# Kernel optimization log

Measured on AMD Instinct MI355X. Metric: run time of the kernel, lower is better.

## Reference

```python
import jax, jax.numpy as jnp
import numpy as np

E, B, D, H, Z = 8, 16384, 512, 512, 64   # experts, batch, input_dim, hidden, latent
NHID = 2                                 # num_mlp_layers - 1 hidden-to-hidden layers


def setup_inputs() -> dict:
    key = jax.random.key(0)
    ks = jax.random.split(key, 12)

    def w(k, shape, fan_in):
        return (jax.random.normal(k, shape, jnp.float32) / np.sqrt(fan_in)).astype(jnp.float32)

    return {
        "x": jax.random.normal(ks[0], (B, D), jnp.float32),
        "eps": jax.random.normal(ks[1], (B, Z), jnp.float32),
        # stacked per-expert parameters (leading axis E)
        "enc_in_w": w(ks[2], (E, D, H), D), "enc_in_b": jnp.zeros((E, H), jnp.float32),
        "enc_hid_w": w(ks[3], (E, NHID, H, H), H), "enc_hid_b": jnp.zeros((E, NHID, H), jnp.float32),
        "mu_w": w(ks[4], (E, H, Z), H), "mu_b": jnp.zeros((E, Z), jnp.float32),
        "lv_w": w(ks[5], (E, H, Z), H), "lv_b": jnp.zeros((E, Z), jnp.float32),
        "dec_in_w": w(ks[6], (E, Z, H), Z), "dec_in_b": jnp.zeros((E, H), jnp.float32),
        "dec_hid_w": w(ks[7], (E, NHID, H, H), H), "dec_hid_b": jnp.zeros((E, NHID, H), jnp.float32),
        "dec_out_w": w(ks[8], (E, H, D), H), "dec_out_b": jnp.zeros((E, D), jnp.float32),
    }


def _moe_forward(x, eps, enc_in_w, enc_in_b, enc_hid_w, enc_hid_b,
                 mu_w, mu_b, lv_w, lv_b,
                 dec_in_w, dec_in_b, dec_hid_w, dec_hid_b, dec_out_w, dec_out_b):
    # ---- every expert tries the problem (dense, all experts over full batch) ----
    h = jax.nn.relu(jnp.einsum('bd,edh->ebh', x, enc_in_w) + enc_in_b[:, None, :])
    for i in range(NHID):
        h = jax.nn.relu(jnp.einsum('ebh,ehk->ebk', h, enc_hid_w[:, i]) + enc_hid_b[:, i, None, :])
    mu = jnp.einsum('ebh,ehz->ebz', h, mu_w) + mu_b[:, None, :]          # [E,B,Z]
    logvar = jnp.einsum('ebh,ehz->ebz', h, lv_w) + lv_b[:, None, :]       # [E,B,Z]
    z = mu + jnp.exp(0.5 * logvar) * eps[None, :, :]                      # reparameterize
    g = jax.nn.relu(jnp.einsum('ebz,ezh->ebh', z, dec_in_w) + dec_in_b[:, None, :])
    for i in range(NHID):
        g = jax.nn.relu(jnp.einsum('ebh,ehk->ebk', g, dec_hid_w[:, i]) + dec_hid_b[:, i, None, :])
    xhat = jnp.einsum('ebh,ehd->ebd', g, dec_out_w) + dec_out_b[:, None, :]  # [E,B,D]

    # ---- per-sample recon loss, pick best expert (torch.min over experts) ----
    recon = jnp.mean((xhat - x[None, :, :]) ** 2, axis=-1)                # [E,B]
    expert_idx = jnp.argmin(recon, axis=0)                                # [B]

    # ---- sparse_others: single fused gather instead of python loop ----
    bi = jnp.arange(x.shape[0])
    return mu[expert_idx, bi], logvar[expert_idx, bi], xhat[expert_idx, bi]


def reference(x, eps, enc_in_w, enc_in_b, enc_hid_w, enc_hid_b,
              mu_w, mu_b, lv_w, lv_b,
              dec_in_w, dec_in_b, dec_hid_w, dec_hid_b, dec_out_w, dec_out_b):
    return _moe_forward(x, eps, enc_in_w, enc_in_b, enc_hid_w, enc_hid_b,
                        mu_w, mu_b, lv_w, lv_b,
                        dec_in_w, dec_in_b, dec_hid_w, dec_hid_b, dec_out_w, dec_out_b)
```

## Files before the change

### kernel.cpp

```cpp
#include <hip/hip_runtime.h>
#include <cstdint>

#define Eexp 8
#define Bb   16384
#define Dd   512
#define Hh   512
#define Zz   64

typedef _Float16 f16x8 __attribute__((ext_vector_type(8)));
typedef float    f32x4 __attribute__((ext_vector_type(4)));

#define OFF_ENCIN  0
#define OFF_HID0   524288
#define OFF_HID1   1048576
#define OFF_HEADS  1572864
#define OFF_DECIN  1703936
#define OFF_DHID0  1769472
#define OFF_DHID1  2293760
#define OFF_DECOUT 2818048
#define PEREXP     3342336
#define WT_TOTAL   (8 * (size_t)PEREXP)

#define GLL16(g, l) __builtin_amdgcn_global_load_lds( \
    (const __attribute__((address_space(1))) void*)(g), \
    (__attribute__((address_space(3))) void*)(l), 16, 0, 0)

template<bool TR>
__global__ __launch_bounds__(256)
void fmsplit(const float* __restrict__ src, _Float16* __restrict__ dst,
             int KTOT, int inner, long sStride, long dStride)
{
    __shared__ float t[64][65];
    const int e  = blockIdx.z;
    const int o0 = blockIdx.x * 64;
    const int k0 = blockIdx.y * 64;
    const float* S = src + (size_t)e * sStride;
    _Float16*    D = dst + (size_t)e * dStride;
    const int tid = threadIdx.x;
    const int rr = tid >> 4, c4 = (tid & 15) * 4;
    #pragma unroll
    for (int p = 0; p < 4; ++p) {
        const int r = rr + p * 16;
        const float4 v = *reinterpret_cast<const float4*>(
            S + (size_t)(TR ? (k0 + r) : (o0 + r)) * inner + (TR ? o0 : k0) + c4);
        t[r][c4 + 0] = v.x; t[r][c4 + 1] = v.y;
        t[r][c4 + 2] = v.z; t[r][c4 + 3] = v.w;
    }
    __syncthreads();
    const int lane = tid & 63, wid = tid >> 6;
    const int KB = KTOT >> 5;
    #pragma unroll
    for (int p = 0; p < 2; ++p) {
        const int g  = wid * 2 + p;
        const int ot = g >> 1, kb = g & 1;
        const int rI = ot * 16 + (lane & 15);
        const int kI = kb * 32 + (lane >> 4) * 8;
        f16x8 hv, lv;
        #pragma unroll
        for (int j = 0; j < 8; ++j) {
            const float v = TR ? t[kI + j][rI] : t[rI][kI + j];
            const _Float16 h = (_Float16)v;
            hv[j] = h; lv[j] = (_Float16)(v - (float)h);
        }
        const size_t base = ((size_t)((o0 >> 4) + ot) * KB + (k0 >> 5) + kb) * 1024;
        *reinterpret_cast<f16x8*>(D + base + lane * 8)       = hv;
        *reinterpret_cast<f16x8*>(D + base + 512 + lane * 8) = lv;
    }
}

__global__ __launch_bounds__(256)
void zfm_kernel(const float* __restrict__ mu, const float* __restrict__ lv,
                const float* __restrict__ eps, _Float16* __restrict__ zfm)
{
    __shared__ float t[64][65];
    const int r0 = blockIdx.x * 64;
    const int tid = threadIdx.x, rr = tid >> 4, c4 = (tid & 15) * 4;
    #pragma unroll
    for (int p = 0; p < 4; ++p) {
        const int r = rr + p * 16;
        const size_t o = (size_t)(r0 + r) * 64 + c4;
        const float4 m = *reinterpret_cast<const float4*>(mu + o);
        const float4 l = *reinterpret_cast<const float4*>(lv + o);
        const float4 e = *reinterpret_cast<const float4*>(eps + o);
        t[r][c4 + 0] = m.x + expf(0.5f * l.x) * e.x;
        t[r][c4 + 1] = m.y + expf(0.5f * l.y) * e.y;
        t[r][c4 + 2] = m.z + expf(0.5f * l.z) * e.z;
        t[r][c4 + 3] = m.w + expf(0.5f * l.w) * e.w;
    }
    __syncthreads();
    const int lane = tid & 63, wid = tid >> 6;
    #pragma unroll
    for (int p = 0; p < 2; ++p) {
        const int g  = wid * 2 + p;
        const int ot = g >> 1, kb = g & 1;
        const int rI = ot * 16 + (lane & 15);
        const int kI = kb * 32 + (lane >> 4) * 8;
        f16x8 hv, lvv;
        #pragma unroll
        for (int j = 0; j < 8; ++j) {
            const float v = t[rI][kI + j];
            const _Float16 h = (_Float16)v;
            hv[j] = h; lvv[j] = (_Float16)(v - (float)h);
        }
        const size_t base = ((size_t)((r0 >> 4) + ot) * 2 + kb) * 1024;
        *reinterpret_cast<f16x8*>(zfm + base + lane * 8)       = hv;
        *reinterpret_cast<f16x8*>(zfm + base + 512 + lane * 8) = lvv;
    }
}

template<int KA, int MODE>
__global__ __launch_bounds__(256, 2)
void gemm9(const _Float16* __restrict__ Afm, const _Float16* __restrict__ Wfm,
           const float* __restrict__ bias0, const float* __restrict__ bias1,
           float* __restrict__ Cf, float* __restrict__ Cf1,
           _Float16* __restrict__ Cfm, const float* __restrict__ Xin,
           float* __restrict__ rec8)
{
    constexpr bool BIG = (MODE != 2);
    constexpr int MF  = BIG ? 4 : 2;
    constexpr int KB  = KA / 32;
    constexpr int NT  = KB;
    constexpr int ACH = BIG ? 16 : 8;
    constexpr int GPW = ACH / 4;
    constexpr int VC  = GPW + 8;
    __shared__ __align__(16) uint8_t smem[BIG ? 32768 : 16384];
    _Float16* ring = reinterpret_cast<_Float16*>(smem);

    const int bid = blockIdx.x;
    int bx, by;
    if (BIG) { const int idx = bid >> 3; bx = (bid & 7) * 16 + (idx >> 2); by = idx & 3; }
    else     { bx = (bid & 7) * 32 + (bid >> 3); by = 0; }

    const int lane = threadIdx.x & 63, wid = threadIdx.x >> 6;
    const int wr = wid >> 1, wc = wid & 1;
    const int row0 = bx * (BIG ? 128 : 64);
    const int col0 = by * 128;
    const int ct0  = (BIG ? (col0 >> 4) : 0) + wc * 4;

    const _Float16* aSrc[GPW];
    #pragma unroll
    for (int p = 0; p < GPW; ++p) {
        const int q = wid * GPW + p;
        aSrc[p] = Afm + (size_t)((row0 >> 4) + (q >> 1)) * KB * 1024
                      + (q & 1) * 512 + lane * 8;
    }
    const _Float16* wSrc[8];
    #pragma unroll
    for (int i = 0; i < 8; ++i)
        wSrc[i] = Wfm + (size_t)(ct0 + (i >> 1)) * KB * 1024
                      + (i & 1) * 512 + lane * 8;

    f32x4 acc[MF][4];
    #pragma unroll
    for (int i = 0; i < MF; ++i)
        #pragma unroll
        for (int j = 0; j < 4; ++j) acc[i][j] = {0.f, 0.f, 0.f, 0.f};

    f16x8 wA[4][2], wB[4][2];

#define STAGE_A(buf)                                                         \
    { _Pragma("unroll")                                                      \
      for (int p = 0; p < GPW; ++p) {                                        \
          GLL16(aSrc[p], ring + (buf) * (ACH * 512) + (wid * GPW + p) * 512);\
          aSrc[p] += 1024;                                                   \
      } }

#define LOAD_W(dst)                                                          \
    { _Pragma("unroll")                                                      \
      for (int i = 0; i < 8; ++i) {                                          \
          dst[i >> 1][i & 1] = *reinterpret_cast<const f16x8*>(wSrc[i]);     \
          wSrc[i] += 1024;                                                   \
      } }

    STAGE_A(0) LOAD_W(wA)
    STAGE_A(1) LOAD_W(wB)

#define ITER(t, buf, wset)                                                   \
    {                                                                        \
        if ((t) + 1 < NT) { asm volatile("s_waitcnt vmcnt(%0)" :: "i"(VC) : "memory"); } \
        else              { asm volatile("s_waitcnt vmcnt(0)" ::: "memory"); } \
        __builtin_amdgcn_s_barrier();                                        \
        asm volatile("" ::: "memory");                                       \
        f16x8 ah[MF], al[MF];                                                \
        _Pragma("unroll")                                                    \
        for (int mf = 0; mf < MF; ++mf) {                                    \
            const int q = (wr * MF + mf) * 2;                                \
            ah[mf] = *reinterpret_cast<const f16x8*>(                        \
                ring + (buf) * (ACH * 512) + q * 512 + lane * 8);            \
            al[mf] = *reinterpret_cast<const f16x8*>(                        \
                ring + (buf) * (ACH * 512) + q * 512 + 512 + lane * 8);      \
        }                                                                    \
        __builtin_amdgcn_s_setprio(1);                                       \
        _Pragma("unroll")                                                    \
        for (int mf = 0; mf < MF; ++mf)                                      \
            _Pragma("unroll")                                                \
            for (int nf = 0; nf < 4; ++nf) {                                 \
                acc[mf][nf] = __builtin_amdgcn_mfma_f32_16x16x32_f16(        \
                    ah[mf], wset[nf][0], acc[mf][nf], 0, 0, 0);              \
                acc[mf][nf] = __builtin_amdgcn_mfma_f32_16x16x32_f16(        \
                    ah[mf], wset[nf][1], acc[mf][nf], 0, 0, 0);              \
                acc[mf][nf] = __builtin_amdgcn_mfma_f32_16x16x32_f16(        \
                    al[mf], wset[nf][0], acc[mf][nf], 0, 0, 0);              \
            }                                                                \
        __builtin_amdgcn_s_setprio(0);                                       \
        if ((t) + 2 < NT) LOAD_W(wset)                                       \
        asm volatile("" ::: "memory");                                       \
        __builtin_amdgcn_s_barrier();                                        \
        asm volatile("" ::: "memory");                                       \
        if ((t) + 2 < NT) STAGE_A(buf)                                       \
    }

    for (int t = 0; t < NT; t += 2) {
        ITER(t,     0, wA)
        ITER(t + 1, 1, wB)
    }
#undef ITER
#undef LOAD_W
#undef STAGE_A

    if constexpr (MODE == 0) {
        uint32_t* sb = reinterpret_cast<uint32_t*>(smem);
        #pragma unroll
        for (int ph = 0; ph < 2; ++ph) {
            if (wc == ph) {
                #pragma unroll
                for (int nf = 0; nf < 4; ++nf) {
                    const int c_l = nf * 16 + (lane & 15);
                    const float bv = bias0[col0 + ph * 64 + c_l];
                    #pragma unroll
                    for (int mf = 0; mf < 4; ++mf)
                        #pragma unroll
                        for (int j = 0; j < 4; ++j) {
                            const int r_l = wr * 64 + mf * 16 + (lane >> 4) * 4 + j;
                            const float v = fmaxf(acc[mf][nf][j] + bv, 0.f);
                            const _Float16 h = (_Float16)v;
                            const _Float16 lo = (_Float16)(v - (float)h);
                            const uint32_t pk =
                                (uint32_t)__builtin_bit_cast(uint16_t, h) |
                                ((uint32_t)__builtin_bit_cast(uint16_t, lo) << 16);
                            sb[r_l * 64 + (((c_l >> 2) ^ (r_l & 15)) << 2) + (c_l & 3)] = pk;
                        }
                }
            }
            __syncthreads();
            {
                #pragma unroll
                for (int i = 0; i < 4; ++i) {
                    const int q = wid * 4 + i;
                    const int T_l = q >> 1, kb_l = q & 1;
                    const int r_l = T_l * 16 + (lane & 15);
                    const int cb  = kb_l * 32 + (lane >> 4) * 8;
                    uint32_t u[8];
                    #pragma unroll
                    for (int jb = 0; jb < 2; ++jb) {
                        const int chunk = ((cb >> 2) + jb) ^ (r_l & 15);
                        const uint32_t* pp = &sb[r_l * 64 + chunk * 4];
                        u[jb*4+0] = pp[0]; u[jb*4+1] = pp[1];
                        u[jb*4+2] = pp[2]; u[jb*4+3] = pp[3];
                    }
                    f16x8 hv, lvv;
                    #pragma unroll
                    for (int j = 0; j < 8; ++j) {
                        hv[j]  = __builtin_bit_cast(_Float16, (uint16_t)(u[j] & 0xffff));
                        lvv[j] = __builtin_bit_cast(_Float16, (uint16_t)(u[j] >> 16));
                    }
                    const size_t base =
                        ((size_t)((row0 >> 4) + T_l) * 16 +
                         ((col0 + ph * 64) >> 5) + kb_l) * 1024;
                    *reinterpret_cast<f16x8*>(Cfm + base + lane * 8)       = hv;
                    *reinterpret_cast<f16x8*>(Cfm + base + 512 + lane * 8) = lvv;
                }
            }
            __syncthreads();
        }
    } else if constexpr (MODE == 1) {
        float rsum[4][4];
        #pragma unroll
        for (int mf = 0; mf < 4; ++mf)
            #pragma unroll
            for (int j = 0; j < 4; ++j) rsum[mf][j] = 0.f;
        #pragma unroll
        for (int nf = 0; nf < 4; ++nf) {
            const int col = col0 + wc * 64 + nf * 16 + (lane & 15);
            const float bv = bias0[col];
            #pragma unroll
            for (int mf = 0; mf < 4; ++mf)
                #pragma unroll
                for (int j = 0; j < 4; ++j) {
                    const int row = row0 + wr * 64 + mf * 16 + (lane >> 4) * 4 + j;
                    const float v = acc[mf][nf][j] + bv;
                    Cf[(size_t)row * 512 + col] = v;
                    const float d = v - Xin[(size_t)row * 512 + col];
                    rsum[mf][j] += d * d;
                }
        }
        #pragma unroll
        for (int mf = 0; mf < 4; ++mf)
            #pragma unroll
            for (int j = 0; j < 4; ++j) {
                float s = rsum[mf][j];
                s += __shfl_xor(s, 1); s += __shfl_xor(s, 2);
                s += __shfl_xor(s, 4); s += __shfl_xor(s, 8);
                if ((lane & 15) == 0) {
                    const int row = row0 + wr * 64 + mf * 16 + (lane >> 4) * 4 + j;
                    rec8[(size_t)(by * 2 + wc) * Bb + row] = s;
                }
            }
    } else {
        #pragma unroll
        for (int nf = 0; nf < 4; ++nf) {
            const int c_h = wc * 64 + nf * 16 + (lane & 15);
            const float bv = (c_h < 64) ? bias0[c_h] : bias1[c_h - 64];
            float* CP = (c_h < 64) ? Cf : Cf1;
            const int c = c_h & 63;
            #pragma unroll
            for (int mf = 0; mf < MF; ++mf)
                #pragma unroll
                for (int j = 0; j < 4; ++j) {
                    const int row = row0 + wr * 32 + mf * 16 + (lane >> 4) * 4 + j;
                    CP[(size_t)row * 64 + c] = acc[mf][nf][j] + bv;
                }
        }
    }
}

__global__ __launch_bounds__(256)
void select_kernel(const float* __restrict__ rec8, float* __restrict__ best,
                   const float* __restrict__ mu_e, const float* __restrict__ lv_e,
                   const float* __restrict__ xhat,
                   float* __restrict__ out_mu, float* __restrict__ out_lv,
                   float* __restrict__ out_xh, int isFirst)
{
    const int wave = threadIdx.x >> 6;
    const int lane = threadIdx.x & 63;
    const int row  = blockIdx.x * 4 + wave;
    float r = 0.f;
    #pragma unroll
    for (int p = 0; p < 8; ++p) r += rec8[(size_t)p * Bb + row];
    r *= (1.0f / 512.0f);
    const bool cond = isFirst || (r < best[row]);
    if (cond) {
        if (lane == 0) best[row] = r;
        out_mu[(size_t)row * Zz + lane] = mu_e[(size_t)row * Zz + lane];
        out_lv[(size_t)row * Zz + lane] = lv_e[(size_t)row * Zz + lane];
        const float4* src = reinterpret_cast<const float4*>(&xhat[(size_t)row * Dd]);
        float4*       dst = reinterpret_cast<float4*>(&out_xh[(size_t)row * Dd]);
        dst[lane]      = src[lane];
        dst[lane + 64] = src[lane + 64];
    }
}

extern "C" void kernel_launch(void* const* d_in, const int* in_sizes, int n_in,
                              void* d_out, int out_size, void* d_ws, size_t ws_size,
                              hipStream_t stream)
{
    const float* x         = (const float*)d_in[0];
    const float* eps       = (const float*)d_in[1];
    const float* enc_in_w  = (const float*)d_in[2];
    const float* enc_in_b  = (const float*)d_in[3];
    const float* enc_hid_w = (const float*)d_in[4];
    const float* enc_hid_b = (const float*)d_in[5];
    const float* mu_w      = (const float*)d_in[6];
    const float* mu_b      = (const float*)d_in[7];
    const float* lv_w      = (const float*)d_in[8];
    const float* lv_b      = (const float*)d_in[9];
    const float* dec_in_w  = (const float*)d_in[10];
    const float* dec_in_b  = (const float*)d_in[11];
    const float* dec_hid_w = (const float*)d_in[12];
    const float* dec_hid_b = (const float*)d_in[13];
    const float* dec_out_w = (const float*)d_in[14];
    const float* dec_out_b = (const float*)d_in[15];

    const size_t FM = (size_t)Bb * 512 * 2;
    const size_t BZ = (size_t)Bb * 64;

    _Float16* wt  = (_Float16*)d_ws;
    _Float16* xfm = wt + WT_TOTAL;
    _Float16* afm = xfm + FM;
    _Float16* bfm = afm + FM;
    _Float16* zfm = bfm + FM;
    float* fbase  = (float*)(zfm + (size_t)Bb * 64 * 2);
    float* xhat   = fbase;
    float* mu_e   = xhat + (size_t)Bb * 512;
    float* lv_e   = mu_e + BZ;
    float* rec8   = lv_e + BZ;
    float* best   = rec8 + (size_t)8 * Bb;

    float* out_mu = (float*)d_out;
    float* out_lv = out_mu + (size_t)Bb * Zz;
    float* out_xh = out_lv + (size_t)Bb * Zz;

    const dim3 blk(256);

    fmsplit<true ><<<dim3(8, 8, 8), blk, 0, stream>>>(enc_in_w,           wt + OFF_ENCIN,  512, 512, 262144, PEREXP);
    fmsplit<true ><<<dim3(8, 8, 8), blk, 0, stream>>>(enc_hid_w,          wt + OFF_HID0,   512, 512, 524288, PEREXP);
    fmsplit<true ><<<dim3(8, 8, 8), blk, 0, stream>>>(enc_hid_w + 262144, wt + OFF_HID1,   512, 512, 524288, PEREXP);
    fmsplit<true ><<<dim3(1, 8, 8), blk, 0, stream>>>(mu_w,               wt + OFF_HEADS,  512,  64,  32768, PEREXP);
    fmsplit<true ><<<dim3(1, 8, 8), blk, 0, stream>>>(lv_w,        wt + OFF_HEADS + 65536, 512,  64,  32768, PEREXP);
    fmsplit<true ><<<dim3(8, 1, 8), blk, 0, stream>>>(dec_in_w,           wt + OFF_DECIN,   64, 512,  32768, PEREXP);
    fmsplit<true ><<<dim3(8, 8, 8), blk, 0, stream>>>(dec_hid_w,          wt + OFF_DHID0,  512, 512, 524288, PEREXP);
    fmsplit<true ><<<dim3(8, 8, 8), blk, 0, stream>>>(dec_hid_w + 262144, wt + OFF_DHID1,  512, 512, 524288, PEREXP);
    fmsplit<true ><<<dim3(8, 8, 8), blk, 0, stream>>>(dec_out_w,          wt + OFF_DECOUT, 512, 512, 262144, PEREXP);
    fmsplit<false><<<dim3(256, 8, 1), blk, 0, stream>>>(x,                xfm,             512, 512, 0, 0);

    const dim3 g512(512), g256(256), gRow(Bb / 4), gZ(Bb / 64);

    for (int e = 0; e < Eexp; ++e) {
        const _Float16* we = wt + (size_t)e * PEREXP;
        gemm9<512, 0><<<g512, blk, 0, stream>>>(
            xfm, we + OFF_ENCIN, enc_in_b + (size_t)e * Hh, nullptr,
            nullptr, nullptr, afm, nullptr, nullptr);
        gemm9<512, 0><<<g512, blk, 0, stream>>>(
            afm, we + OFF_HID0, enc_hid_b + ((size_t)e * 2 + 0) * Hh, nullptr,
            nullptr, nullptr, bfm, nullptr, nullptr);
        gemm9<512, 0><<<g512, blk, 0, stream>>>(
            bfm, we + OFF_HID1, enc_hid_b + ((size_t)e * 2 + 1) * Hh, nullptr,
            nullptr, nullptr, afm, nullptr, nullptr);
        gemm9<512, 2><<<g256, blk, 0, stream>>>(
            afm, we + OFF_HEADS, mu_b + (size_t)e * Zz, lv_b + (size_t)e * Zz,
            mu_e, lv_e, nullptr, nullptr, nullptr);
        zfm_kernel<<<gZ, blk, 0, stream>>>(mu_e, lv_e, eps, zfm);
        gemm9< 64, 0><<<g512, blk, 0, stream>>>(
            zfm, we + OFF_DECIN, dec_in_b + (size_t)e * Hh, nullptr,
            nullptr, nullptr, bfm, nullptr, nullptr);
        gemm9<512, 0><<<g512, blk, 0, stream>>>(
            bfm, we + OFF_DHID0, dec_hid_b + ((size_t)e * 2 + 0) * Hh, nullptr,
            nullptr, nullptr, afm, nullptr, nullptr);
        gemm9<512, 0><<<g512, blk, 0, stream>>>(
            afm, we + OFF_DHID1, dec_hid_b + ((size_t)e * 2 + 1) * Hh, nullptr,
            nullptr, nullptr, bfm, nullptr, nullptr);
        gemm9<512, 1><<<g512, blk, 0, stream>>>(
            bfm, we + OFF_DECOUT, dec_out_b + (size_t)e * Dd, nullptr,
            xhat, nullptr, nullptr, x, rec8);
        select_kernel<<<gRow, blk, 0, stream>>>(
            rec8, best, mu_e, lv_e, xhat, out_mu, out_lv, out_xh, e == 0 ? 1 : 0);
    }
}
```

Baseline: 1.814 ms.

## Load GEMM A fragments directly into registers, dropping LDS staging and barriers

The GEMM main loop no longer stages A tiles through LDS with global_load_lds and per-step barriers. Each wave now loads its own A and W fragments straight from global memory into registers, double-buffered, with no block synchronisation in the K loop. The block-to-tile mapping is also reordered. This removes the LDS round-trip and barrier stalls, but A data shared between the two column waves is now fetched twice from global/L2, and register pressure rises.

New measurement: 2.690 ms. 48.3% more time.

```diff
diff --git a/kernel.cpp b/kernel.cpp
--- a/kernel.cpp
+++ b/kernel.cpp
@@ -20,10 +20,6 @@
 #define OFF_DECOUT 2818048
 #define PEREXP     3342336
 #define WT_TOTAL   (8 * (size_t)PEREXP)
-
-#define GLL16(g, l) __builtin_amdgcn_global_load_lds( \
-    (const __attribute__((address_space(1))) void*)(g), \
-    (__attribute__((address_space(3))) void*)(l), 16, 0, 0)
 
 template<bool TR>
 __global__ __launch_bounds__(256)
@@ -110,25 +106,21 @@
 
 template<int KA, int MODE>
 __global__ __launch_bounds__(256, 2)
-void gemm9(const _Float16* __restrict__ Afm, const _Float16* __restrict__ Wfm,
-           const float* __restrict__ bias0, const float* __restrict__ bias1,
-           float* __restrict__ Cf, float* __restrict__ Cf1,
-           _Float16* __restrict__ Cfm, const float* __restrict__ Xin,
-           float* __restrict__ rec8)
+void gemm10(const _Float16* __restrict__ Afm, const _Float16* __restrict__ Wfm,
+            const float* __restrict__ bias0, const float* __restrict__ bias1,
+            float* __restrict__ Cf, float* __restrict__ Cf1,
+            _Float16* __restrict__ Cfm, const float* __restrict__ Xin,
+            float* __restrict__ rec8)
 {
     constexpr bool BIG = (MODE != 2);
-    constexpr int MF  = BIG ? 4 : 2;
-    constexpr int KB  = KA / 32;
-    constexpr int NT  = KB;
-    constexpr int ACH = BIG ? 16 : 8;
-    constexpr int GPW = ACH / 4;
-    constexpr int VC  = GPW + 8;
-    __shared__ __align__(16) uint8_t smem[BIG ? 32768 : 16384];
-    _Float16* ring = reinterpret_cast<_Float16*>(smem);
+    constexpr int MF = BIG ? 4 : 2;
+    constexpr int KB = KA / 32;
+    constexpr int NT = KB;
+    __shared__ __align__(16) uint8_t smem[(MODE == 0) ? 32768 : 64];
 
     const int bid = blockIdx.x;
     int bx, by;
-    if (BIG) { const int idx = bid >> 3; bx = (bid & 7) * 16 + (idx >> 2); by = idx & 3; }
+    if (BIG) { bx = (bid & 7) * 16 + (bid >> 5); by = (bid >> 3) & 3; }
     else     { bx = (bid & 7) * 32 + (bid >> 3); by = 0; }
 
     const int lane = threadIdx.x & 63, wid = threadIdx.x >> 6;
@@ -137,18 +129,16 @@
     const int col0 = by * 128;
     const int ct0  = (BIG ? (col0 >> 4) : 0) + wc * 4;
 
-    const _Float16* aSrc[GPW];
-    #pragma unroll
-    for (int p = 0; p < GPW; ++p) {
-        const int q = wid * GPW + p;
-        aSrc[p] = Afm + (size_t)((row0 >> 4) + (q >> 1)) * KB * 1024
-                      + (q & 1) * 512 + lane * 8;
-    }
-    const _Float16* wSrc[8];
+    const _Float16* aP[2 * MF];
+    #pragma unroll
+    for (int i = 0; i < 2 * MF; ++i)
+        aP[i] = Afm + (size_t)((row0 >> 4) + wr * MF + (i >> 1)) * KB * 1024
+                    + (i & 1) * 512 + lane * 8;
+    const _Float16* wP[8];
     #pragma unroll
     for (int i = 0; i < 8; ++i)
-        wSrc[i] = Wfm + (size_t)(ct0 + (i >> 1)) * KB * 1024
-                      + (i & 1) * 512 + lane * 8;
+        wP[i] = Wfm + (size_t)(ct0 + (i >> 1)) * KB * 1024
+                    + (i & 1) * 512 + lane * 8;
 
     f32x4 acc[MF][4];
     #pragma unroll
@@ -156,67 +146,45 @@
         #pragma unroll
         for (int j = 0; j < 4; ++j) acc[i][j] = {0.f, 0.f, 0.f, 0.f};
 
-    f16x8 wA[4][2], wB[4][2];
-
-#define STAGE_A(buf)                                                         \
+    f16x8 fa0[MF][2], fa1[MF][2], fw0[4][2], fw1[4][2];
+
+#define LDA(dst)                                                             \
     { _Pragma("unroll")                                                      \
-      for (int p = 0; p < GPW; ++p) {                                        \
-          GLL16(aSrc[p], ring + (buf) * (ACH * 512) + (wid * GPW + p) * 512);\
-          aSrc[p] += 1024;                                                   \
+      for (int i = 0; i < 2 * MF; ++i) {                                     \
+          dst[i >> 1][i & 1] = *reinterpret_cast<const f16x8*>(aP[i]);       \
+          aP[i] += 1024;                                                     \
       } }
-
-#define LOAD_W(dst)                                                          \
+#define LDW(dst)                                                             \
     { _Pragma("unroll")                                                      \
       for (int i = 0; i < 8; ++i) {                                          \
-          dst[i >> 1][i & 1] = *reinterpret_cast<const f16x8*>(wSrc[i]);     \
-          wSrc[i] += 1024;                                                   \
+          dst[i >> 1][i & 1] = *reinterpret_cast<const f16x8*>(wP[i]);       \
+          wP[i] += 1024;                                                     \
       } }
-
-    STAGE_A(0) LOAD_W(wA)
-    STAGE_A(1) LOAD_W(wB)
-
-#define ITER(t, buf, wset)                                                   \
-    {                                                                        \
-        if ((t) + 1 < NT) { asm volatile("s_waitcnt vmcnt(%0)" :: "i"(VC) : "memory"); } \
-        else              { asm volatile("s_waitcnt vmcnt(0)" ::: "memory"); } \
-        __builtin_amdgcn_s_barrier();                                        \
-        asm volatile("" ::: "memory");                                       \
-        f16x8 ah[MF], al[MF];                                                \
-        _Pragma("unroll")                                                    \
-        for (int mf = 0; mf < MF; ++mf) {                                    \
-            const int q = (wr * MF + mf) * 2;                                \
-            ah[mf] = *reinterpret_cast<const f16x8*>(                        \
-                ring + (buf) * (ACH * 512) + q * 512 + lane * 8);            \
-            al[mf] = *reinterpret_cast<const f16x8*>(                        \
-                ring + (buf) * (ACH * 512) + q * 512 + 512 + lane * 8);      \
-        }                                                                    \
-        __builtin_amdgcn_s_setprio(1);                                       \
-        _Pragma("unroll")                                                    \
-        for (int mf = 0; mf < MF; ++mf)                                      \
-            _Pragma("unroll")                                                \
-            for (int nf = 0; nf < 4; ++nf) {                                 \
-                acc[mf][nf] = __builtin_amdgcn_mfma_f32_16x16x32_f16(        \
-                    ah[mf], wset[nf][0], acc[mf][nf], 0, 0, 0);              \
-                acc[mf][nf] = __builtin_amdgcn_mfma_f32_16x16x32_f16(        \
-                    ah[mf], wset[nf][1], acc[mf][nf], 0, 0, 0);              \
-                acc[mf][nf] = __builtin_amdgcn_mfma_f32_16x16x32_f16(        \
-                    al[mf], wset[nf][0], acc[mf][nf], 0, 0, 0);              \
-            }                                                                \
-        __builtin_amdgcn_s_setprio(0);                                       \
-        if ((t) + 2 < NT) LOAD_W(wset)                                       \
-        asm volatile("" ::: "memory");                                       \
-        __builtin_amdgcn_s_barrier();                                        \
-        asm volatile("" ::: "memory");                                       \
-        if ((t) + 2 < NT) STAGE_A(buf)                                       \
-    }
+#define MM(fa, fw)                                                           \
+    { _Pragma("unroll")                                                      \
+      for (int mf = 0; mf < MF; ++mf)                                        \
+          _Pragma("unroll")                                                  \
+          for (int nf = 0; nf < 4; ++nf) {                                   \
+              acc[mf][nf] = __builtin_amdgcn_mfma_f32_16x16x32_f16(          \
+                  fa[mf][0], fw[nf][0], acc[mf][nf], 0, 0, 0);               \
+              acc[mf][nf] = __builtin_amdgcn_mfma_f32_16x16x32_f16(          \
+                  fa[mf][0], fw[nf][1], acc[mf][nf], 0, 0, 0);               \
+              acc[mf][nf] = __builtin_amdgcn_mfma_f32_16x16x32_f16(          \
+                  fa[mf][1], fw[nf][0], acc[mf][nf], 0, 0, 0);               \
+          } }
+
+    LDA(fa0) LDW(fw0)
+    if (NT > 1) { LDA(fa1) LDW(fw1) }
 
     for (int t = 0; t < NT; t += 2) {
-        ITER(t,     0, wA)
-        ITER(t + 1, 1, wB)
-    }
-#undef ITER
-#undef LOAD_W
-#undef STAGE_A
+        MM(fa0, fw0)
+        if (t + 2 < NT) { LDA(fa0) LDW(fw0) }
+        MM(fa1, fw1)
+        if (t + 3 < NT) { LDA(fa1) LDW(fw1) }
+    }
+#undef MM
+#undef LDW
+#undef LDA
 
     if constexpr (MODE == 0) {
         uint32_t* sb = reinterpret_cast<uint32_t*>(smem);
@@ -407,29 +375,29 @@
 
     for (int e = 0; e < Eexp; ++e) {
         const _Float16* we = wt + (size_t)e * PEREXP;
-        gemm9<512, 0><<<g512, blk, 0, stream>>>(
+        gemm10<512, 0><<<g512, blk, 0, stream>>>(
             xfm, we + OFF_ENCIN, enc_in_b + (size_t)e * Hh, nullptr,
             nullptr, nullptr, afm, nullptr, nullptr);
-        gemm9<512, 0><<<g512, blk, 0, stream>>>(
+        gemm10<512, 0><<<g512, blk, 0, stream>>>(
             afm, we + OFF_HID0, enc_hid_b + ((size_t)e * 2 + 0) * Hh, nullptr,
             nullptr, nullptr, bfm, nullptr, nullptr);
-        gemm9<512, 0><<<g512, blk, 0, stream>>>(
+        gemm10<512, 0><<<g512, blk, 0, stream>>>(
             bfm, we + OFF_HID1, enc_hid_b + ((size_t)e * 2 + 1) * Hh, nullptr,
             nullptr, nullptr, afm, nullptr, nullptr);
-        gemm9<512, 2><<<g256, blk, 0, stream>>>(
+        gemm10<512, 2><<<g256, blk, 0, stream>>>(
             afm, we + OFF_HEADS, mu_b + (size_t)e * Zz, lv_b + (size_t)e * Zz,
             mu_e, lv_e, nullptr, nullptr, nullptr);
         zfm_kernel<<<gZ, blk, 0, stream>>>(mu_e, lv_e, eps, zfm);
-        gemm9< 64, 0><<<g512, blk, 0, stream>>>(
+        gemm10< 64, 0><<<g512, blk, 0, stream>>>(
             zfm, we + OFF_DECIN, dec_in_b + (size_t)e * Hh, nullptr,
             nullptr, nullptr, bfm, nullptr, nullptr);
-        gemm9<512, 0><<<g512, blk, 0, stream>>>(
+        gemm10<512, 0><<<g512, blk, 0, stream>>>(
             bfm, we + OFF_DHID0, dec_hid_b + ((size_t)e * 2 + 0) * Hh, nullptr,
             nullptr, nullptr, afm, nullptr, nullptr);
-        gemm9<512, 0><<<g512, blk, 0, stream>>>(
+        gemm10<512, 0><<<g512, blk, 0, stream>>>(
             afm, we + OFF_DHID1, dec_hid_b + ((size_t)e * 2 + 1) * Hh, nullptr,
             nullptr, nullptr, bfm, nullptr, nullptr);
-        gemm9<512, 1><<<g512, blk, 0, stream>>>(
+        gemm10<512, 1><<<g512, blk, 0, stream>>>(
             bfm, we + OFF_DECOUT, dec_out_b + (size_t)e * Dd, nullptr,
             xhat, nullptr, nullptr, x, rec8);
         select_kernel<<<gRow, blk, 0, stream>>>(
```
